# Kernel optimization log

Measured on AMD Instinct MI355X. Metric: run time of the kernel, lower is better.

## Reference

```python
import jax, jax.numpy as jnp
import numpy as np

S, B, E, H = 2048, 2, 1024, 16
D = E // H  # head_dim = 64


def setup_inputs() -> dict:
    key = jax.random.key(0)
    ks = jax.random.split(key, 5)
    sp = (2.0 / (E + E)) ** 0.5  # xavier-ish scale
    return {
        "x": jax.random.normal(ks[0], (S, B, E), dtype=jnp.float32),
        "wq": jax.random.normal(ks[1], (E, E), dtype=jnp.float32) * sp,
        "bq": jnp.zeros((E,), jnp.float32),
        "wk": jax.random.normal(ks[2], (E, E), dtype=jnp.float32) * sp,
        "bk": jnp.zeros((E,), jnp.float32),
        "wv": jax.random.normal(ks[3], (E, E), dtype=jnp.float32) * sp,
        "bv": jnp.zeros((E,), jnp.float32),
        "wo": jax.random.normal(ks[4], (E, E), dtype=jnp.float32) * sp,
        "bo": jnp.zeros((E,), jnp.float32),
    }


def reference(x, wq, bq, wk, bk, wv, bv, wo, bo):
    # x: (S, B, E), weights in torch Linear convention (out, in)
    scaling = jnp.float32(D ** -0.5)
    q = (jnp.einsum('ibe,fe->ibf', x, wq) + bq) * scaling
    k = jnp.einsum('ibe,fe->ibf', x, wk) + bk
    v = jnp.einsum('ibe,fe->ibf', x, wv) + bv
    q = q.reshape(S, B, H, D)
    k = k.reshape(S, B, H, D)
    v = v.reshape(S, B, H, D)
    # energy: (B, H, S_q, S_k)
    energy = jnp.einsum('ibnf,jbnf->bnij', q, k)
    causal = jnp.triu(jnp.ones((S, S), dtype=bool), k=1)  # True above diagonal
    energy = jnp.where(causal[None, None], -jnp.inf, energy)
    weights = jax.nn.softmax(energy, axis=-1)
    head_ctx = jnp.einsum('bnij,jbnf->ibnf', weights, v)
    context = head_ctx.reshape(S, B, E)
    out = jnp.einsum('ibe,fe->ibf', context, wo) + bo
    return out
```

## Files before the change

### kernel.cpp

```cpp
#include <hip/hip_runtime.h>
#include <hip/hip_bf16.h>
#include <stdint.h>

#define S_LEN 2048
#define BATCH 2
#define EMB   1024
#define NH    16
#define HD    64
#define LOG2E 1.4426950408889634f

typedef __bf16 bf16x8 __attribute__((ext_vector_type(8)));
typedef float  f32x4  __attribute__((ext_vector_type(4)));
typedef unsigned short ushort8 __attribute__((ext_vector_type(8)));

__device__ __forceinline__ unsigned short f2bf(float f) {
  __bf16 h = (__bf16)f;
  return __builtin_bit_cast(unsigned short, h);
}

__device__ __forceinline__ ushort8 cvt8(const float4 a, const float4 b) {
  ushort8 o;
  o[0]=f2bf(a.x); o[1]=f2bf(a.y); o[2]=f2bf(a.z); o[3]=f2bf(a.w);
  o[4]=f2bf(b.x); o[5]=f2bf(b.y); o[6]=f2bf(b.z); o[7]=f2bf(b.w);
  return o;
}

__device__ __forceinline__ unsigned long long pack4(const f32x4 v) {
  return  (unsigned long long)f2bf(v[0])
       | ((unsigned long long)f2bf(v[1]) << 16)
       | ((unsigned long long)f2bf(v[2]) << 32)
       | ((unsigned long long)f2bf(v[3]) << 48);
}

#define GLOAD16(g, l) __builtin_amdgcn_global_load_lds( \
    (const __attribute__((address_space(1))) void*)(g),  \
    (__attribute__((address_space(3))) void*)(l), 16, 0, 0)

__global__ __launch_bounds__(256) void k_cvt(const float* __restrict__ src,
                                             unsigned short* __restrict__ dst,
                                             int n) {
  int i = (blockIdx.x*256 + threadIdx.x)*8;
  if (i >= n) return;
  const float4* s4 = (const float4*)(src + i);
  *(ushort8*)(dst + i) = cvt8(s4[0], s4[1]);
}

__global__ __launch_bounds__(256) void k_cvt_all(
    const float* __restrict__ x,
    const float* __restrict__ wq, const float* __restrict__ wk,
    const float* __restrict__ wv,
    unsigned short* __restrict__ xb, unsigned short* __restrict__ wb) {
  const int b = blockIdx.x;
  const float* src;
  unsigned short* dst;
  int off;
  if (b < 2048) { src = x; dst = xb; off = b; }
  else {
    const int t = b - 2048;
    const int z = t >> 9;
    src = (z==0) ? wq : ((z==1) ? wk : wv);
    dst = wb + (size_t)z*EMB*EMB;
    off = t & 511;
  }
  const int i = (off*256 + threadIdx.x)*8;
  const float4* s4 = (const float4*)(src + i);
  *(ushort8*)(dst + i) = cvt8(s4[0], s4[1]);
}

__global__ __launch_bounds__(256) void k_qkv_bb(
    const unsigned short* __restrict__ xb,
    const unsigned short* __restrict__ wb,
    const float* __restrict__ bq, const float* __restrict__ bk,
    const float* __restrict__ bv,
    unsigned short* __restrict__ Qb, unsigned short* __restrict__ Kb,
    unsigned short* __restrict__ Vtb)
{
  __shared__ unsigned short Al[2][128*32];
  __shared__ unsigned short Bl[2][128*32];
  const int tid = threadIdx.x;
  const int lin  = blockIdx.x;
  const int wgid = (lin & 7)*96 + (lin >> 3);
  const int mb   = wgid / 24;
  const int t    = wgid % 24;
  const int z    = t >> 3;
  const int nb   = t & 7;
  const int m0 = mb * 128;
  const int n0 = nb * 128;
  const int w = tid >> 6, lane = tid & 63;
  const int wr = w >> 1, wc = w & 1;
  const int lr = lane & 15, lhi = lane >> 4;
  const unsigned short* wz = wb + (size_t)z * (EMB*EMB);

  const unsigned short* ag[2];
  const unsigned short* bg[2];
  int ub[2];
#pragma unroll
  for (int j=0;j<2;++j) {
    const int c   = j*256 + tid;
    const int row = c >> 2;
    const int col = (c & 3) << 3;
    ag[j] = xb + (size_t)(m0+row)*EMB + col;
    bg[j] = wz + (size_t)(n0+row)*EMB + col;
    ub[j] = (j*256 + (tid & 192)) * 16;
  }

  auto STAGE = [&](int k0, int b2) {
#pragma unroll
    for (int j=0;j<2;++j) {
      GLOAD16(ag[j] + k0, (char*)Al[b2] + ub[j]);
      GLOAD16(bg[j] + k0, (char*)Bl[b2] + ub[j]);
    }
  };

  f32x4 acc[4][4];
#pragma unroll
  for (int m=0;m<4;++m)
#pragma unroll
    for (int n=0;n<4;++n) acc[m][n] = (f32x4){0.f,0.f,0.f,0.f};

  STAGE(0, 0);
  int bbuf = 0;
  for (int k0 = 0; k0 < EMB; k0 += 32) {
    if (k0 + 32 < EMB) {
      STAGE(k0 + 32, bbuf^1);
      asm volatile("s_waitcnt vmcnt(4)" ::: "memory");
    } else {
      asm volatile("s_waitcnt vmcnt(0)" ::: "memory");
    }
    __builtin_amdgcn_s_barrier();

    bf16x8 af[4], bfr[4];
#pragma unroll
    for (int m=0;m<4;++m) af[m]  = *(const bf16x8*)&Al[bbuf][(wr*64 + m*16 + lr)*32 + lhi*8];
#pragma unroll
    for (int n=0;n<4;++n) bfr[n] = *(const bf16x8*)&Bl[bbuf][(wc*64 + n*16 + lr)*32 + lhi*8];
    __builtin_amdgcn_s_setprio(1);
#pragma unroll
    for (int m=0;m<4;++m)
#pragma unroll
      for (int n=0;n<4;++n)
        acc[m][n] = __builtin_amdgcn_mfma_f32_16x16x32_bf16(af[m], bfr[n], acc[m][n], 0,0,0);
    __builtin_amdgcn_s_setprio(0);

    __builtin_amdgcn_s_barrier();
    bbuf ^= 1;
  }

  const float scale = (z==0) ? 0.125f*LOG2E : 1.0f;
  const float* bias = (z==0) ? bq : ((z==1) ? bk : bv);
#pragma unroll
  for (int m=0;m<4;++m)
#pragma unroll
    for (int n=0;n<4;++n)
#pragma unroll
      for (int r=0;r<4;++r) {
        const int rr   = m0 + wr*64 + m*16 + lhi*4 + r;
        const int fcol = n0 + wc*64 + n*16 + lr;
        const float v = (acc[m][n][r] + bias[fcol]) * scale;
        const unsigned short ov = f2bf(v);
        const int i = rr >> 1, bsel = rr & 1;
        const int h = fcol >> 6, d = fcol & 63;
        const int hh = bsel*NH + h;
        if (z == 0)      Qb [((size_t)hh*S_LEN + i)*HD + d] = ov;
        else if (z == 1) Kb [((size_t)hh*S_LEN + i)*HD + d] = ov;
        else             Vtb[((size_t)hh*HD + d)*S_LEN + i] = ov;
      }
}

__global__ __launch_bounds__(256) void k_qkv_bf(
    const unsigned short* __restrict__ xb,
    const float* __restrict__ wq, const float* __restrict__ wk,
    const float* __restrict__ wv,
    const float* __restrict__ bq, const float* __restrict__ bk,
    const float* __restrict__ bv,
    unsigned short* __restrict__ Qb, unsigned short* __restrict__ Kb,
    unsigned short* __restrict__ Vtb)
{
  __shared__ unsigned short Al[128*32];
  __shared__ unsigned short Bl[128*32];
  const int tid = threadIdx.x;
  const int lin  = blockIdx.x;
  const int wgid = (lin & 7)*96 + (lin >> 3);
  const int mb   = wgid / 24;
  const int t    = wgid % 24;
  const int z    = t >> 3;
  const int nb   = t & 7;
  const int m0 = mb * 128;
  const int n0 = nb * 128;
  const int w = tid >> 6, lane = tid & 63;
  const int wr = w >> 1, wc = w & 1;
  const int lr = lane & 15, lhi = lane >> 4;
  const float* wz = (z==0) ? wq : ((z==1) ? wk : wv);

  f32x4 acc[4][4];
#pragma unroll
  for (int m=0;m<4;++m)
#pragma unroll
    for (int n=0;n<4;++n) acc[m][n] = (f32x4){0.f,0.f,0.f,0.f};

  for (int k0 = 0; k0 < EMB; k0 += 32) {
    float4 b0[2], b1[2];
#pragma unroll
    for (int j = 0; j < 2; ++j) {
      const int c   = j*256 + tid;
      const int row = c >> 2;
      const int col = (c & 3) << 3;
      const float* bp = wz + (size_t)(n0+row)*EMB + k0 + col;
      b0[j] = *(const float4*)bp;  b1[j] = *(const float4*)(bp+4);
    }
    __syncthreads();
#pragma unroll
    for (int j = 0; j < 2; ++j) {
      const int c   = j*256 + tid;
      const int row = c >> 2;
      const int col = (c & 3) << 3;
      const int ub  = (j*256 + (tid & 192)) * 16;
      GLOAD16(xb + (size_t)(m0+row)*EMB + k0 + col, (char*)Al + ub);
      *(ushort8*)&Bl[row*32 + col] = cvt8(b0[j], b1[j]);
    }
    __syncthreads();
    bf16x8 af[4], bfr[4];
#pragma unroll
    for (int m=0;m<4;++m) af[m]  = *(const bf16x8*)&Al[(wr*64 + m*16 + lr)*32 + lhi*8];
#pragma unroll
    for (int n=0;n<4;++n) bfr[n] = *(const bf16x8*)&Bl[(wc*64 + n*16 + lr)*32 + lhi*8];
#pragma unroll
    for (int m=0;m<4;++m)
#pragma unroll
      for (int n=0;n<4;++n)
        acc[m][n] = __builtin_amdgcn_mfma_f32_16x16x32_bf16(af[m], bfr[n], acc[m][n], 0,0,0);
  }

  const float scale = (z==0) ? 0.125f*LOG2E : 1.0f;
  const float* bias = (z==0) ? bq : ((z==1) ? bk : bv);
#pragma unroll
  for (int m=0;m<4;++m)
#pragma unroll
    for (int n=0;n<4;++n)
#pragma unroll
      for (int r=0;r<4;++r) {
        const int rr   = m0 + wr*64 + m*16 + lhi*4 + r;
        const int fcol = n0 + wc*64 + n*16 + lr;
        const float v = (acc[m][n][r] + bias[fcol]) * scale;
        const unsigned short ov = f2bf(v);
        const int i = rr >> 1, bsel = rr & 1;
        const int h = fcol >> 6, d = fcol & 63;
        const int hh = bsel*NH + h;
        if (z == 0)      Qb [((size_t)hh*S_LEN + i)*HD + d] = ov;
        else if (z == 1) Kb [((size_t)hh*S_LEN + i)*HD + d] = ov;
        else             Vtb[((size_t)hh*HD + d)*S_LEN + i] = ov;
      }
}

__global__ __launch_bounds__(256) void k_qkv(
    const float* __restrict__ xA, int a_rs, int ishift,
    const float* __restrict__ wq, const float* __restrict__ wk,
    const float* __restrict__ wv,
    const float* __restrict__ bq, const float* __restrict__ bk,
    const float* __restrict__ bv,
    unsigned short* __restrict__ Qb, unsigned short* __restrict__ Kb,
    unsigned short* __restrict__ Vtb)
{
  __shared__ unsigned short Al[128*32];
  __shared__ unsigned short Bl[128*32];
  const int tid = threadIdx.x;
  const int z  = blockIdx.z;
  const int m0 = blockIdx.x * 128;
  const int n0 = blockIdx.y * 128;
  const int w = tid >> 6, lane = tid & 63;
  const int wr = w >> 1, wc = w & 1;
  const int lr = lane & 15, lhi = lane >> 4;
  const float* wz = (z==0) ? wq : ((z==1) ? wk : wv);

  f32x4 acc[4][4];
#pragma unroll
  for (int m=0;m<4;++m)
#pragma unroll
    for (int n=0;n<4;++n) acc[m][n] = (f32x4){0.f,0.f,0.f,0.f};

  for (int k0 = 0; k0 < EMB; k0 += 32) {
    float4 a0[2], a1[2], b0[2], b1[2];
#pragma unroll
    for (int j = 0; j < 2; ++j) {
      const int c   = j*256 + tid;
      const int row = c >> 2;
      const int col = (c & 3) << 3;
      const float* ap = xA + (size_t)(m0+row)*a_rs + k0 + col;
      const float* bp = wz + (size_t)(n0+row)*EMB + k0 + col;
      a0[j] = *(const float4*)ap;  a1[j] = *(const float4*)(ap+4);
      b0[j] = *(const float4*)bp;  b1[j] = *(const float4*)(bp+4);
    }
    __syncthreads();
#pragma unroll
    for (int j = 0; j < 2; ++j) {
      const int c   = j*256 + tid;
      const int row = c >> 2;
      const int col = (c & 3) << 3;
      *(ushort8*)&Al[row*32 + col] = cvt8(a0[j], a1[j]);
      *(ushort8*)&Bl[row*32 + col] = cvt8(b0[j], b1[j]);
    }
    __syncthreads();
    bf16x8 af[4], bfr[4];
#pragma unroll
    for (int m=0;m<4;++m) af[m]  = *(const bf16x8*)&Al[(wr*64 + m*16 + lr)*32 + lhi*8];
#pragma unroll
    for (int n=0;n<4;++n) bfr[n] = *(const bf16x8*)&Bl[(wc*64 + n*16 + lr)*32 + lhi*8];
#pragma unroll
    for (int m=0;m<4;++m)
#pragma unroll
      for (int n=0;n<4;++n)
        acc[m][n] = __builtin_amdgcn_mfma_f32_16x16x32_bf16(af[m], bfr[n], acc[m][n], 0,0,0);
  }

  const float scale = (z==0) ? 0.125f*LOG2E : 1.0f;
  const float* bias = (z==0) ? bq : ((z==1) ? bk : bv);
  const int bmask = (1 << ishift) - 1;
#pragma unroll
  for (int m=0;m<4;++m)
#pragma unroll
    for (int n=0;n<4;++n)
#pragma unroll
      for (int r=0;r<4;++r) {
        const int rr   = m0 + wr*64 + m*16 + lhi*4 + r;
        const int fcol = n0 + wc*64 + n*16 + lr;
        const float v = (acc[m][n][r] + bias[fcol]) * scale;
        const unsigned short ov = f2bf(v);
        const int i = rr >> ishift, bsel = rr & bmask;
        const int h = fcol >> 6, d = fcol & 63;
        const int hh = bsel*NH + h;
        if (z == 0)      Qb [((size_t)hh*S_LEN + i)*HD + d] = ov;
        else if (z == 1) Kb [((size_t)hh*S_LEN + i)*HD + d] = ov;
        else             Vtb[((size_t)hh*HD + d)*S_LEN + i] = ov;
      }
}

__global__ __launch_bounds__(256,4) void k_attn(
    const unsigned short* __restrict__ Q,
    const unsigned short* __restrict__ K,
    const unsigned short* __restrict__ Vt,
    unsigned short* __restrict__ ctx, int bshift, int hsh)
{
  __shared__ unsigned short KL[2][64*64];
  __shared__ unsigned short VL[2][64*64];
  __shared__ unsigned short Pl[4][16*64];

  const int tid = threadIdx.x;
  const int w = tid >> 6, lane = tid & 63;
  const int lr = lane & 15, lhi = lane >> 4;

  const int lin = blockIdx.x;
  const int cc  = lin >> hsh;
  const int chunk = (cc < 16) ? cc : (47 - cc);
  const int hh  = lin & ((1 << hsh) - 1);
  const int q0  = chunk*64 + w*16;

  const unsigned short* Qh = Q  + (size_t)hh*S_LEN*HD;
  const unsigned short* Kh = K  + (size_t)hh*S_LEN*HD;
  const unsigned short* Vh = Vt + (size_t)hh*HD*S_LEN;
  char* Pw = (char*)Pl[w];

  const int xm = (lr & 7) << 4;
  int kvb[2];
#pragma unroll
  for (int kf=0;kf<2;++kf) kvb[kf] = lr*128 + ((kf*64 + lhi*16) ^ xm);
  int pwb[4];
#pragma unroll
  for (int kn=0;kn<4;++kn)
    pwb[kn] = lr*128 + ((kn*32 + lhi*8) ^ xm);

  const unsigned short* kga[2];
  const unsigned short* vga[2];
#pragma unroll
  for (int j=0;j<2;++j) {
    const int c   = j*256 + tid;
    const int row = c >> 3;
    const int sb  = (c*16) ^ ((row & 7) << 4);
    const int el  = (sb & 127) >> 1;
    kga[j] = Kh + (size_t)row*HD + el;
    vga[j] = Vh + (size_t)row*S_LEN + el;
  }
  const int ub0 = (tid & 192) * 16;

  bf16x8 qf[2];
#pragma unroll
  for (int kf=0;kf<2;++kf)
    qf[kf] = *(const bf16x8*)&Qh[(size_t)(q0 + lr)*HD + kf*32 + lhi*8];

  f32x4 o[4];
  float rm = -3.0e38f, rl = 0.f;
#pragma unroll
  for (int dn=0;dn<4;++dn) o[dn] = (f32x4){0.f,0.f,0.f,0.f};

  const int tmax = chunk + 1;

  auto STAGE = [&](int tt, int bb2) {
#pragma unroll
    for (int j=0;j<2;++j) {
      GLOAD16(kga[j] + (size_t)tt*4096, (char*)KL[bb2] + ub0 + j*4096);
      GLOAD16(vga[j] + (size_t)tt*64,   (char*)VL[bb2] + ub0 + j*4096);
    }
  };

  STAGE(0, 0);
  int bb = 0;
  for (int t = 0; t < tmax; ++t) {
    if (t + 1 < tmax) {
      STAGE(t+1, bb^1);
      asm volatile("s_waitcnt vmcnt(4)" ::: "memory");
    } else {
      asm volatile("s_waitcnt vmcnt(0)" ::: "memory");
    }
    __builtin_amdgcn_s_barrier();

    const int kv0 = t*64;
    const char* KB = (const char*)KL[bb];
    const char* VB = (const char*)VL[bb];

    f32x4 st[4];
#pragma unroll
    for (int kn=0;kn<4;++kn) st[kn] = (f32x4){0.f,0.f,0.f,0.f};

    __builtin_amdgcn_s_setprio(1);
#pragma unroll
    for (int kn=0;kn<4;++kn)
#pragma unroll
      for (int kf=0;kf<2;++kf) {
        const bf16x8 kfr = *(const bf16x8*)(KB + kvb[kf] + kn*2048);
        st[kn] = __builtin_amdgcn_mfma_f32_16x16x32_bf16(kfr, qf[kf], st[kn], 0,0,0);
      }
    __builtin_amdgcn_s_setprio(0);

    if (t == tmax-1) {
      const int q = q0 + lr;
#pragma unroll
      for (int kn=0;kn<4;++kn)
#pragma unroll
        for (int r=0;r<4;++r) {
          const int k = kv0 + kn*16 + lhi*4 + r;
          if (k > q) st[kn][r] = -1.0e30f;
        }
    }

    float mx = fmaxf(fmaxf(st[0][0], st[0][1]), fmaxf(st[0][2], st[0][3]));
#pragma unroll
    for (int kn=1;kn<4;++kn)
      mx = fmaxf(mx, fmaxf(fmaxf(st[kn][0], st[kn][1]),
                           fmaxf(st[kn][2], st[kn][3])));
    mx = fmaxf(mx, __shfl_xor(mx, 16));
    mx = fmaxf(mx, __shfl_xor(mx, 32));
    if (!__all(mx - rm <= 8.0f)) {
      const float newm  = fmaxf(rm, mx);
      const float alpha = exp2f(rm - newm);
      rl *= alpha;
#pragma unroll
      for (int dn=0;dn<4;++dn)
#pragma unroll
        for (int r=0;r<4;++r) o[dn][r] *= alpha;
      rm = newm;
    }
    float sum = 0.f;
#pragma unroll
    for (int kn=0;kn<4;++kn)
#pragma unroll
      for (int r=0;r<4;++r) {
        const float p = exp2f(st[kn][r] - rm);
        st[kn][r] = p;
        sum += p;
      }
    sum += __shfl_xor(sum, 16);
    sum += __shfl_xor(sum, 32);
    rl += sum;

#pragma unroll
    for (int kn=0;kn<4;++kn)
      *(unsigned long long*)(Pw + pwb[kn]) = pack4(st[kn]);

#pragma unroll
    for (int ks=0;ks<2;++ks) {
      const bf16x8 pfr = *(const bf16x8*)(Pw + kvb[ks]);
      __builtin_amdgcn_s_setprio(1);
#pragma unroll
      for (int dn=0;dn<4;++dn) {
        const bf16x8 vf = *(const bf16x8*)(VB + kvb[ks] + dn*2048);
        o[dn] = __builtin_amdgcn_mfma_f32_16x16x32_bf16(vf, pfr, o[dn], 0,0,0);
      }
      __builtin_amdgcn_s_setprio(0);
    }

    __builtin_amdgcn_s_barrier();
    bb ^= 1;
  }

  const int h = hh & (NH-1);
  const int badd = hh >> 4;
  const float inv = 1.0f / rl;
  const int q = q0 + lr;
  const size_t trow = ((size_t)q << bshift) + badd;
#pragma unroll
  for (int dn=0;dn<4;++dn) {
    f32x4 ov;
#pragma unroll
    for (int r=0;r<4;++r) ov[r] = o[dn][r]*inv;
    *(unsigned long long*)&ctx[trow*EMB + h*HD + dn*16 + lhi*4] = pack4(ov);
  }
}

__global__ __launch_bounds__(256) void k_oproj_bf(
    const unsigned short* __restrict__ ctxA,
    const unsigned short* __restrict__ wob,
    const float* __restrict__ bo,
    float* __restrict__ out)
{
  __shared__ unsigned short Al[2][128*32];
  __shared__ unsigned short Bl[2][128*32];
  const int tid = threadIdx.x;
  const int m0 = blockIdx.x * 128;
  const int n0 = blockIdx.y * 128;
  const int w = tid >> 6, lane = tid & 63;
  const int wr = w >> 1, wc = w & 1;
  const int lr = lane & 15, lhi = lane >> 4;

  const unsigned short* ag[2];
  const unsigned short* bg[2];
  int ub[2];
#pragma unroll
  for (int j=0;j<2;++j) {
    const int c   = j*256 + tid;
    const int row = c >> 2;
    const int col = (c & 3) << 3;
    ag[j] = ctxA + (size_t)(m0+row)*EMB + col;
    bg[j] = wob  + (size_t)(n0+row)*EMB + col;
    ub[j] = (j*256 + (tid & 192)) * 16;
  }

  auto STAGE = [&](int k0, int b2) {
#pragma unroll
    for (int j=0;j<2;++j) {
      GLOAD16(ag[j] + k0, (char*)Al[b2] + ub[j]);
      GLOAD16(bg[j] + k0, (char*)Bl[b2] + ub[j]);
    }
  };

  f32x4 acc[4][4];
#pragma unroll
  for (int m=0;m<4;++m)
#pragma unroll
    for (int n=0;n<4;++n) acc[m][n] = (f32x4){0.f,0.f,0.f,0.f};

  STAGE(0, 0);
  int bbuf = 0;
  for (int k0 = 0; k0 < EMB; k0 += 32) {
    if (k0 + 32 < EMB) {
      STAGE(k0 + 32, bbuf^1);
      asm volatile("s_waitcnt vmcnt(4)" ::: "memory");
    } else {
      asm volatile("s_waitcnt vmcnt(0)" ::: "memory");
    }
    __builtin_amdgcn_s_barrier();

    bf16x8 af[4], bfr[4];
#pragma unroll
    for (int m=0;m<4;++m) af[m]  = *(const bf16x8*)&Al[bbuf][(wr*64 + m*16 + lr)*32 + lhi*8];
#pragma unroll
    for (int n=0;n<4;++n) bfr[n] = *(const bf16x8*)&Bl[bbuf][(wc*64 + n*16 + lr)*32 + lhi*8];
    __builtin_amdgcn_s_setprio(1);
#pragma unroll
    for (int m=0;m<4;++m)
#pragma unroll
      for (int n=0;n<4;++n)
        acc[m][n] = __builtin_amdgcn_mfma_f32_16x16x32_bf16(af[m], bfr[n], acc[m][n], 0,0,0);
    __builtin_amdgcn_s_setprio(0);

    __builtin_amdgcn_s_barrier();
    bbuf ^= 1;
  }

#pragma unroll
  for (int m=0;m<4;++m)
#pragma unroll
    for (int n=0;n<4;++n)
#pragma unroll
      for (int r=0;r<4;++r) {
        const int rr   = m0 + wr*64 + m*16 + lhi*4 + r;
        const int fcol = n0 + wc*64 + n*16 + lr;
        out[(size_t)rr*EMB + fcol] = acc[m][n][r] + bo[fcol];
      }
}

__global__ __launch_bounds__(256) void k_oproj(
    const unsigned short* __restrict__ ctxA,
    const float* __restrict__ wo,
    const float* __restrict__ bo,
    float* __restrict__ outb, int orm)
{
  __shared__ unsigned short Al[128*32];
  __shared__ unsigned short Bl[128*32];
  const int tid = threadIdx.x;
  const int m0 = blockIdx.x * 128;
  const int n0 = blockIdx.y * 128;
  const int w = tid >> 6, lane = tid & 63;
  const int wr = w >> 1, wc = w & 1;
  const int lr = lane & 15, lhi = lane >> 4;

  f32x4 acc[4][4];
#pragma unroll
  for (int m=0;m<4;++m)
#pragma unroll
    for (int n=0;n<4;++n) acc[m][n] = (f32x4){0.f,0.f,0.f,0.f};

  for (int k0 = 0; k0 < EMB; k0 += 32) {
    float4 b0[2], b1[2];
#pragma unroll
    for (int j = 0; j < 2; ++j) {
      const int c   = j*256 + tid;
      const int row = c >> 2;
      const int col = (c & 3) << 3;
      const float* bp = wo + (size_t)(n0+row)*EMB + k0 + col;
      b0[j] = *(const float4*)bp;  b1[j] = *(const float4*)(bp+4);
    }
    __syncthreads();
#pragma unroll
    for (int j = 0; j < 2; ++j) {
      const int c   = j*256 + tid;
      const int row = c >> 2;
      const int col = (c & 3) << 3;
      const int ub  = (j*256 + (tid & 192)) * 16;
      GLOAD16(ctxA + (size_t)(m0+row)*EMB + k0 + col, (char*)Al + ub);
      *(ushort8*)&Bl[row*32 + col] = cvt8(b0[j], b1[j]);
    }
    __syncthreads();
    bf16x8 af[4], bfr[4];
#pragma unroll
    for (int m=0;m<4;++m) af[m]  = *(const bf16x8*)&Al[(wr*64 + m*16 + lr)*32 + lhi*8];
#pragma unroll
    for (int n=0;n<4;++n) bfr[n] = *(const bf16x8*)&Bl[(wc*64 + n*16 + lr)*32 + lhi*8];
#pragma unroll
    for (int m=0;m<4;++m)
#pragma unroll
      for (int n=0;n<4;++n)
        acc[m][n] = __builtin_amdgcn_mfma_f32_16x16x32_bf16(af[m], bfr[n], acc[m][n], 0,0,0);
  }

#pragma unroll
  for (int m=0;m<4;++m)
#pragma unroll
    for (int n=0;n<4;++n)
#pragma unroll
      for (int r=0;r<4;++r) {
        const int rr   = m0 + wr*64 + m*16 + lhi*4 + r;
        const int fcol = n0 + wc*64 + n*16 + lr;
        outb[(size_t)rr*orm*EMB + fcol] = acc[m][n][r] + bo[fcol];
      }
}

extern "C" void kernel_launch(void* const* d_in, const int* in_sizes, int n_in,
                              void* d_out, int out_size, void* d_ws, size_t ws_size,
                              hipStream_t stream) {
  const float* x  = (const float*)d_in[0];
  const float* wq = (const float*)d_in[1];
  const float* bq = (const float*)d_in[2];
  const float* wk = (const float*)d_in[3];
  const float* bk = (const float*)d_in[4];
  const float* wv = (const float*)d_in[5];
  const float* bv = (const float*)d_in[6];
  const float* wo = (const float*)d_in[7];
  const float* bo = (const float*)d_in[8];
  float* out = (float*)d_out;

  char* ws = (char*)d_ws;
  const size_t MB = (size_t)1 << 20;

  if (ws_size >= 38*MB) {
    unsigned short* Q   = (unsigned short*)(ws + 0*MB);
    unsigned short* K   = (unsigned short*)(ws + 8*MB);
    unsigned short* Vt  = (unsigned short*)(ws + 16*MB);
    unsigned short* wb  = (unsigned short*)(ws + 24*MB);
    unsigned short* xb  = (unsigned short*)(ws + 30*MB);
    unsigned short* cx  = (unsigned short*)(ws + 24*MB);
    unsigned short* wob = Vt;

    k_cvt_all<<<3584, 256, 0, stream>>>(x, wq, wk, wv, xb, wb);
    k_qkv_bb<<<768, 256, 0, stream>>>(xb, wb, bq,bk,bv, Q, K, Vt);
    k_attn<<<1024, 256, 0, stream>>>(Q, K, Vt, cx, 1, 5);
    k_cvt<<<512, 256, 0, stream>>>(wo, wob, EMB*EMB);
    k_oproj_bf<<<dim3(32,8), 256, 0, stream>>>(cx, wob, bo, out);
  } else if (ws_size >= 32*MB) {
    unsigned short* Q   = (unsigned short*)(ws + 0*MB);
    unsigned short* K   = (unsigned short*)(ws + 8*MB);
    unsigned short* Vt  = (unsigned short*)(ws + 16*MB);
    unsigned short* cx  = (unsigned short*)(ws + 24*MB);
    unsigned short* xb  = cx;
    unsigned short* wob = Vt;

    k_cvt<<<2048, 256, 0, stream>>>(x, xb, (S_LEN*BATCH)*EMB);
    k_qkv_bf<<<768, 256, 0, stream>>>(xb, wq,wk,wv, bq,bk,bv, Q, K, Vt);
    k_attn<<<1024, 256, 0, stream>>>(Q, K, Vt, cx, 1, 5);
    k_cvt<<<512, 256, 0, stream>>>(wo, wob, EMB*EMB);
    k_oproj_bf<<<dim3(32,8), 256, 0, stream>>>(cx, wob, bo, out);
  } else {
    unsigned short* Q  = (unsigned short*)(ws + 0*MB);
    unsigned short* K  = (unsigned short*)(ws + 4*MB);
    unsigned short* Vt = (unsigned short*)(ws + 8*MB);
    unsigned short* cx = (unsigned short*)(ws + 12*MB);
    for (int b = 0; b < 2; ++b) {
      k_qkv<<<dim3(16,8,3), 256, 0, stream>>>(x + b*EMB, 2*EMB, 0,
                                              wq,wk,wv, bq,bk,bv, Q,K,Vt);
      k_attn<<<512, 256, 0, stream>>>(Q, K, Vt, cx, 0, 4);
      k_oproj<<<dim3(16,8), 256, 0, stream>>>(cx, wo, bo, out + b*EMB, 2);
    }
  }
}
```

Before: 126.4 us.

## Split long causal attention chunks across two KV halves with a combine pass

The attention kernel is replaced by a variant that splits the KV range of the later query chunks into two halves handled by separate blocks. It stores a normalized partial output plus running max/sum statistics, and a new combine kernel merges the halves into the context buffer. This shortens the longest per-block tile loop and evens out per-block work under the causal mask. The cost is an extra kernel launch, extra global traffic for the partials, and a bf16 rounding of the partial outputs before the merge.

Measured after the change: 132.2 us. +4.5%, slower.

```diff
diff --git a/kernel.cpp b/kernel.cpp
--- a/kernel.cpp
+++ b/kernel.cpp
@@ -16,6 +16,9 @@
 __device__ __forceinline__ unsigned short f2bf(float f) {
   __bf16 h = (__bf16)f;
   return __builtin_bit_cast(unsigned short, h);
+}
+__device__ __forceinline__ float bf2f(unsigned short u) {
+  return (float)__builtin_bit_cast(__bf16, u);
 }
 
 __device__ __forceinline__ ushort8 cvt8(const float4 a, const float4 b) {
@@ -334,7 +337,224 @@
       }
 }
 
-__global__ __launch_bounds__(256,4) void k_attn(
+__global__ __launch_bounds__(256,4) void k_attn_j(
+    const unsigned short* __restrict__ Q,
+    const unsigned short* __restrict__ K,
+    const unsigned short* __restrict__ Vt,
+    unsigned short* __restrict__ ctx,
+    unsigned short* __restrict__ PA,
+    float2* __restrict__ mlA, float2* __restrict__ mlB)
+{
+  __shared__ unsigned short KL[2][64*64];
+  __shared__ unsigned short VL[2][64*64];
+  __shared__ unsigned short Pl[4][16*64];
+
+  const int tid = threadIdx.x;
+  const int w = tid >> 6, lane = tid & 63;
+  const int lr = lane & 15, lhi = lane >> 4;
+
+  const int j  = blockIdx.x >> 5;
+  const int hh = blockIdx.x & 31;
+  int c, ts, nt, mode;
+  if (j < 16)      { c = 31-j; ts = (c+1)>>1; nt = (c+1)-ts; mode = 2; }
+  else if (j < 32) { c = 47-j; ts = 0;        nt = (c+1)>>1; mode = 1; }
+  else             { c = 47-j; ts = 0;        nt = c+1;      mode = 0; }
+  const bool diag = (mode != 1);
+  const int q0 = c*64 + w*16;
+
+  const unsigned short* Qh = Q  + (size_t)hh*S_LEN*HD;
+  const unsigned short* Kh = K  + (size_t)hh*S_LEN*HD;
+  const unsigned short* Vh = Vt + (size_t)hh*HD*S_LEN;
+  char* Pw = (char*)Pl[w];
+
+  const int xm = (lr & 7) << 4;
+  int kvb[2];
+#pragma unroll
+  for (int kf=0;kf<2;++kf) kvb[kf] = lr*128 + ((kf*64 + lhi*16) ^ xm);
+  int pwb[4];
+#pragma unroll
+  for (int kn=0;kn<4;++kn)
+    pwb[kn] = lr*128 + ((kn*32 + lhi*8) ^ xm);
+
+  const unsigned short* kga[2];
+  const unsigned short* vga[2];
+#pragma unroll
+  for (int jj=0;jj<2;++jj) {
+    const int cc  = jj*256 + tid;
+    const int row = cc >> 3;
+    const int sb  = (cc*16) ^ ((row & 7) << 4);
+    const int el  = (sb & 127) >> 1;
+    kga[jj] = Kh + (size_t)row*HD + el;
+    vga[jj] = Vh + (size_t)row*S_LEN + el;
+  }
+  const int ub0 = (tid & 192) * 16;
+
+  bf16x8 qf[2];
+#pragma unroll
+  for (int kf=0;kf<2;++kf)
+    qf[kf] = *(const bf16x8*)&Qh[(size_t)(q0 + lr)*HD + kf*32 + lhi*8];
+
+  f32x4 o[4];
+  float rm = -3.0e38f, rl = 0.f;
+#pragma unroll
+  for (int dn=0;dn<4;++dn) o[dn] = (f32x4){0.f,0.f,0.f,0.f};
+
+  auto STAGE = [&](int tt, int bb2) {
+#pragma unroll
+    for (int jj=0;jj<2;++jj) {
+      GLOAD16(kga[jj] + (size_t)tt*4096, (char*)KL[bb2] + ub0 + jj*4096);
+      GLOAD16(vga[jj] + (size_t)tt*64,   (char*)VL[bb2] + ub0 + jj*4096);
+    }
+  };
+
+  STAGE(ts, 0);
+  int bb = 0;
+  for (int i = 0; i < nt; ++i) {
+    const int t = ts + i;
+    if (i + 1 < nt) {
+      STAGE(t+1, bb^1);
+      asm volatile("s_waitcnt vmcnt(4)" ::: "memory");
+    } else {
+      asm volatile("s_waitcnt vmcnt(0)" ::: "memory");
+    }
+    __builtin_amdgcn_s_barrier();
+
+    const int kv0 = t*64;
+    const char* KB = (const char*)KL[bb];
+    const char* VB = (const char*)VL[bb];
+
+    f32x4 st[4];
+#pragma unroll
+    for (int kn=0;kn<4;++kn) st[kn] = (f32x4){0.f,0.f,0.f,0.f};
+
+    __builtin_amdgcn_s_setprio(1);
+#pragma unroll
+    for (int kn=0;kn<4;++kn)
+#pragma unroll
+      for (int kf=0;kf<2;++kf) {
+        const bf16x8 kfr = *(const bf16x8*)(KB + kvb[kf] + kn*2048);
+        st[kn] = __builtin_amdgcn_mfma_f32_16x16x32_bf16(kfr, qf[kf], st[kn], 0,0,0);
+      }
+    __builtin_amdgcn_s_setprio(0);
+
+    if (diag && i == nt-1) {
+      const int qr = q0 + lr;
+#pragma unroll
+      for (int kn=0;kn<4;++kn)
+#pragma unroll
+        for (int r=0;r<4;++r) {
+          const int k = kv0 + kn*16 + lhi*4 + r;
+          if (k > qr) st[kn][r] = -1.0e30f;
+        }
+    }
+
+    float mx = fmaxf(fmaxf(st[0][0], st[0][1]), fmaxf(st[0][2], st[0][3]));
+#pragma unroll
+    for (int kn=1;kn<4;++kn)
+      mx = fmaxf(mx, fmaxf(fmaxf(st[kn][0], st[kn][1]),
+                           fmaxf(st[kn][2], st[kn][3])));
+    mx = fmaxf(mx, __shfl_xor(mx, 16));
+    mx = fmaxf(mx, __shfl_xor(mx, 32));
+    if (!__all(mx - rm <= 8.0f)) {
+      const float newm  = fmaxf(rm, mx);
+      const float alpha = exp2f(rm - newm);
+      rl *= alpha;
+#pragma unroll
+      for (int dn=0;dn<4;++dn)
+#pragma unroll
+        for (int r=0;r<4;++r) o[dn][r] *= alpha;
+      rm = newm;
+    }
+    float sum = 0.f;
+#pragma unroll
+    for (int kn=0;kn<4;++kn)
+#pragma unroll
+      for (int r=0;r<4;++r) {
+        const float p = exp2f(st[kn][r] - rm);
+        st[kn][r] = p;
+        sum += p;
+      }
+    sum += __shfl_xor(sum, 16);
+    sum += __shfl_xor(sum, 32);
+    rl += sum;
+
+#pragma unroll
+    for (int kn=0;kn<4;++kn)
+      *(unsigned long long*)(Pw + pwb[kn]) = pack4(st[kn]);
+
+#pragma unroll
+    for (int ks=0;ks<2;++ks) {
+      const bf16x8 pfr = *(const bf16x8*)(Pw + kvb[ks]);
+      __builtin_amdgcn_s_setprio(1);
+#pragma unroll
+      for (int dn=0;dn<4;++dn) {
+        const bf16x8 vf = *(const bf16x8*)(VB + kvb[ks] + dn*2048);
+        o[dn] = __builtin_amdgcn_mfma_f32_16x16x32_bf16(vf, pfr, o[dn], 0,0,0);
+      }
+      __builtin_amdgcn_s_setprio(0);
+    }
+
+    __builtin_amdgcn_s_barrier();
+    bb ^= 1;
+  }
+
+  const float inv = 1.0f / rl;
+  const int qr = q0 + lr;
+  if (mode == 1) {
+    unsigned short* pb = PA + (((size_t)hh << 10) + (qr - 1024))*64;
+#pragma unroll
+    for (int dn=0;dn<4;++dn) {
+      f32x4 ov;
+#pragma unroll
+      for (int r=0;r<4;++r) ov[r] = o[dn][r]*inv;
+      *(unsigned long long*)(pb + dn*16 + lhi*4) = pack4(ov);
+    }
+    if (lhi == 0) mlA[((size_t)hh << 10) + (qr - 1024)] = make_float2(rm, rl);
+  } else {
+    const int h = hh & (NH-1);
+    const int badd = hh >> 4;
+    const size_t trow = ((size_t)qr << 1) + badd;
+#pragma unroll
+    for (int dn=0;dn<4;++dn) {
+      f32x4 ov;
+#pragma unroll
+      for (int r=0;r<4;++r) ov[r] = o[dn][r]*inv;
+      *(unsigned long long*)&ctx[trow*EMB + h*HD + dn*16 + lhi*4] = pack4(ov);
+    }
+    if (mode == 2 && lhi == 0)
+      mlB[((size_t)hh << 10) + (qr - 1024)] = make_float2(rm, rl);
+  }
+}
+
+__global__ __launch_bounds__(256) void k_comb(
+    const unsigned short* __restrict__ PA,
+    const float2* __restrict__ mlA, const float2* __restrict__ mlB,
+    unsigned short* __restrict__ ctx)
+{
+  const int gid = blockIdx.x*256 + threadIdx.x;
+  const int hh  = gid >> 13;
+  const int rem = gid & 8191;
+  const int q   = rem >> 3;
+  const int d0  = (rem & 7) << 3;
+  const float2 A = mlA[((size_t)hh << 10) + q];
+  const float2 B = mlB[((size_t)hh << 10) + q];
+  const float m  = fmaxf(A.x, B.x);
+  float wA = exp2f(A.x - m) * A.y;
+  float wB = exp2f(B.x - m) * B.y;
+  const float inv = 1.0f / (wA + wB);
+  wA *= inv;  wB *= inv;
+  const ushort8 a8 = *(const ushort8*)&PA[((((size_t)hh << 10) + q) << 6) + d0];
+  const size_t trow = (size_t)(1024 + q)*2 + (hh >> 4);
+  unsigned short* cp = ctx + trow*EMB + (hh & 15)*HD + d0;
+  const ushort8 b8 = *(const ushort8*)cp;
+  ushort8 r;
+#pragma unroll
+  for (int i=0;i<8;++i)
+    r[i] = f2bf(bf2f(a8[i])*wA + bf2f(b8[i])*wB);
+  *(ushort8*)cp = r;
+}
+
+__global__ __launch_bounds__(256,4) void k_attn_u(
     const unsigned short* __restrict__ Q,
     const unsigned short* __restrict__ K,
     const unsigned short* __restrict__ Vt,
@@ -677,11 +897,15 @@
     unsigned short* wb  = (unsigned short*)(ws + 24*MB);
     unsigned short* xb  = (unsigned short*)(ws + 30*MB);
     unsigned short* cx  = (unsigned short*)(ws + 24*MB);
+    unsigned short* PA  = (unsigned short*)(ws + 32*MB);
+    float2*         mlA = (float2*)(ws + 36*MB);
+    float2*         mlB = (float2*)(ws + 36*MB + 256*1024);
     unsigned short* wob = Vt;
 
     k_cvt_all<<<3584, 256, 0, stream>>>(x, wq, wk, wv, xb, wb);
     k_qkv_bb<<<768, 256, 0, stream>>>(xb, wb, bq,bk,bv, Q, K, Vt);
-    k_attn<<<1024, 256, 0, stream>>>(Q, K, Vt, cx, 1, 5);
+    k_attn_j<<<1536, 256, 0, stream>>>(Q, K, Vt, cx, PA, mlA, mlB);
+    k_comb<<<1024, 256, 0, stream>>>(PA, mlA, mlB, cx);
     k_cvt<<<512, 256, 0, stream>>>(wo, wob, EMB*EMB);
     k_oproj_bf<<<dim3(32,8), 256, 0, stream>>>(cx, wob, bo, out);
   } else if (ws_size >= 32*MB) {
@@ -694,7 +918,7 @@
 
     k_cvt<<<2048, 256, 0, stream>>>(x, xb, (S_LEN*BATCH)*EMB);
     k_qkv_bf<<<768, 256, 0, stream>>>(xb, wq,wk,wv, bq,bk,bv, Q, K, Vt);
-    k_attn<<<1024, 256, 0, stream>>>(Q, K, Vt, cx, 1, 5);
+    k_attn_u<<<1024, 256, 0, stream>>>(Q, K, Vt, cx, 1, 5);
     k_cvt<<<512, 256, 0, stream>>>(wo, wob, EMB*EMB);
     k_oproj_bf<<<dim3(32,8), 256, 0, stream>>>(cx, wob, bo, out);
   } else {
@@ -705,7 +929,7 @@
     for (int b = 0; b < 2; ++b) {
       k_qkv<<<dim3(16,8,3), 256, 0, stream>>>(x + b*EMB, 2*EMB, 0,
                                               wq,wk,wv, bq,bk,bv, Q,K,Vt);
-      k_attn<<<512, 256, 0, stream>>>(Q, K, Vt, cx, 0, 4);
+      k_attn_u<<<512, 256, 0, stream>>>(Q, K, Vt, cx, 0, 4);
       k_oproj<<<dim3(16,8), 256, 0, stream>>>(cx, wo, bo, out + b*EMB, 2);
     }
   }
```

## Fold wo conversion into cvt_all and defer softmax row-sum reduction

Applied to the files above, without the earlier changes.

Adds a 40MB workspace path where the wo weight conversion is folded into the single k_cvt_all launch, writing to its own buffer so one kernel launch is removed. In the attention kernel, the per-tile cross-lane shuffle reduction of the softmax denominator moves to after the loop, with each lane accumulating a partial sum. The max reduction is reshaped into four independent chains, and the bf16 pack now builds 32-bit halves instead of a 64-bit value. This relies on the per-lane partial sums staying consistent under the alpha rescaling, which holds because alpha is wave-uniform.

Result: faster. 122.5 us (-3.1%).

```diff
diff --git a/kernel.cpp b/kernel.cpp
--- a/kernel.cpp
+++ b/kernel.cpp
@@ -25,11 +25,11 @@
   return o;
 }
 
-__device__ __forceinline__ unsigned long long pack4(const f32x4 v) {
-  return  (unsigned long long)f2bf(v[0])
-       | ((unsigned long long)f2bf(v[1]) << 16)
-       | ((unsigned long long)f2bf(v[2]) << 32)
-       | ((unsigned long long)f2bf(v[3]) << 48);
+__device__ __forceinline__ uint2 pack4(const f32x4 v) {
+  uint2 r;
+  r.x = (unsigned)f2bf(v[0]) | ((unsigned)f2bf(v[1]) << 16);
+  r.y = (unsigned)f2bf(v[2]) | ((unsigned)f2bf(v[3]) << 16);
+  return r;
 }
 
 #define GLOAD16(g, l) __builtin_amdgcn_global_load_lds( \
@@ -48,8 +48,9 @@
 __global__ __launch_bounds__(256) void k_cvt_all(
     const float* __restrict__ x,
     const float* __restrict__ wq, const float* __restrict__ wk,
-    const float* __restrict__ wv,
-    unsigned short* __restrict__ xb, unsigned short* __restrict__ wb) {
+    const float* __restrict__ wv, const float* __restrict__ wo,
+    unsigned short* __restrict__ xb, unsigned short* __restrict__ wb,
+    unsigned short* __restrict__ wob) {
   const int b = blockIdx.x;
   const float* src;
   unsigned short* dst;
@@ -58,8 +59,8 @@
   else {
     const int t = b - 2048;
     const int z = t >> 9;
-    src = (z==0) ? wq : ((z==1) ? wk : wv);
-    dst = wb + (size_t)z*EMB*EMB;
+    if (z < 3) { src = (z==0) ? wq : ((z==1) ? wk : wv); dst = wb + (size_t)z*EMB*EMB; }
+    else       { src = wo; dst = wob; }
     off = t & 511;
   }
   const int i = (off*256 + threadIdx.x)*8;
@@ -334,7 +335,7 @@
       }
 }
 
-__global__ __launch_bounds__(256,4) void k_attn(
+__global__ __launch_bounds__(256,4) void k_attn_u(
     const unsigned short* __restrict__ Q,
     const unsigned short* __restrict__ K,
     const unsigned short* __restrict__ Vt,
@@ -441,11 +442,11 @@
         }
     }
 
-    float mx = fmaxf(fmaxf(st[0][0], st[0][1]), fmaxf(st[0][2], st[0][3]));
-#pragma unroll
-    for (int kn=1;kn<4;++kn)
-      mx = fmaxf(mx, fmaxf(fmaxf(st[kn][0], st[kn][1]),
-                           fmaxf(st[kn][2], st[kn][3])));
+    float t0 = fmaxf(fmaxf(fmaxf(st[0][0], st[0][1]), st[0][2]), st[0][3]);
+    float t1 = fmaxf(fmaxf(fmaxf(st[1][0], st[1][1]), st[1][2]), st[1][3]);
+    float t2 = fmaxf(fmaxf(fmaxf(st[2][0], st[2][1]), st[2][2]), st[2][3]);
+    float t3 = fmaxf(fmaxf(fmaxf(st[3][0], st[3][1]), st[3][2]), st[3][3]);
+    float mx = fmaxf(fmaxf(fmaxf(t0, t1), t2), t3);
     mx = fmaxf(mx, __shfl_xor(mx, 16));
     mx = fmaxf(mx, __shfl_xor(mx, 32));
     if (!__all(mx - rm <= 8.0f)) {
@@ -458,22 +459,18 @@
         for (int r=0;r<4;++r) o[dn][r] *= alpha;
       rm = newm;
     }
-    float sum = 0.f;
 #pragma unroll
     for (int kn=0;kn<4;++kn)
 #pragma unroll
       for (int r=0;r<4;++r) {
         const float p = exp2f(st[kn][r] - rm);
         st[kn][r] = p;
-        sum += p;
+        rl += p;
       }
-    sum += __shfl_xor(sum, 16);
-    sum += __shfl_xor(sum, 32);
-    rl += sum;
 
 #pragma unroll
     for (int kn=0;kn<4;++kn)
-      *(unsigned long long*)(Pw + pwb[kn]) = pack4(st[kn]);
+      *(uint2*)(Pw + pwb[kn]) = pack4(st[kn]);
 
 #pragma unroll
     for (int ks=0;ks<2;++ks) {
@@ -491,6 +488,8 @@
     bb ^= 1;
   }
 
+  rl += __shfl_xor(rl, 16);
+  rl += __shfl_xor(rl, 32);
   const int h = hh & (NH-1);
   const int badd = hh >> 4;
   const float inv = 1.0f / rl;
@@ -501,7 +500,7 @@
     f32x4 ov;
 #pragma unroll
     for (int r=0;r<4;++r) ov[r] = o[dn][r]*inv;
-    *(unsigned long long*)&ctx[trow*EMB + h*HD + dn*16 + lhi*4] = pack4(ov);
+    *(uint2*)&ctx[trow*EMB + h*HD + dn*16 + lhi*4] = pack4(ov);
   }
 }
 
@@ -670,7 +669,20 @@
   char* ws = (char*)d_ws;
   const size_t MB = (size_t)1 << 20;
 
-  if (ws_size >= 38*MB) {
+  if (ws_size >= 40*MB) {
+    unsigned short* Q   = (unsigned short*)(ws + 0*MB);
+    unsigned short* K   = (unsigned short*)(ws + 8*MB);
+    unsigned short* Vt  = (unsigned short*)(ws + 16*MB);
+    unsigned short* wb  = (unsigned short*)(ws + 24*MB);
+    unsigned short* xb  = (unsigned short*)(ws + 30*MB);
+    unsigned short* wob = (unsigned short*)(ws + 38*MB);
+    unsigned short* cx  = (unsigned short*)(ws + 24*MB);
+
+    k_cvt_all<<<4096, 256, 0, stream>>>(x, wq, wk, wv, wo, xb, wb, wob);
+    k_qkv_bb<<<768, 256, 0, stream>>>(xb, wb, bq,bk,bv, Q, K, Vt);
+    k_attn_u<<<1024, 256, 0, stream>>>(Q, K, Vt, cx, 1, 5);
+    k_oproj_bf<<<dim3(32,8), 256, 0, stream>>>(cx, wob, bo, out);
+  } else if (ws_size >= 38*MB) {
     unsigned short* Q   = (unsigned short*)(ws + 0*MB);
     unsigned short* K   = (unsigned short*)(ws + 8*MB);
     unsigned short* Vt  = (unsigned short*)(ws + 16*MB);
@@ -679,9 +691,9 @@
     unsigned short* cx  = (unsigned short*)(ws + 24*MB);
     unsigned short* wob = Vt;
 
-    k_cvt_all<<<3584, 256, 0, stream>>>(x, wq, wk, wv, xb, wb);
+    k_cvt_all<<<3584, 256, 0, stream>>>(x, wq, wk, wv, wo, xb, wb, (unsigned short*)0);
     k_qkv_bb<<<768, 256, 0, stream>>>(xb, wb, bq,bk,bv, Q, K, Vt);
-    k_attn<<<1024, 256, 0, stream>>>(Q, K, Vt, cx, 1, 5);
+    k_attn_u<<<1024, 256, 0, stream>>>(Q, K, Vt, cx, 1, 5);
     k_cvt<<<512, 256, 0, stream>>>(wo, wob, EMB*EMB);
     k_oproj_bf<<<dim3(32,8), 256, 0, stream>>>(cx, wob, bo, out);
   } else if (ws_size >= 32*MB) {
@@ -694,7 +706,7 @@
 
     k_cvt<<<2048, 256, 0, stream>>>(x, xb, (S_LEN*BATCH)*EMB);
     k_qkv_bf<<<768, 256, 0, stream>>>(xb, wq,wk,wv, bq,bk,bv, Q, K, Vt);
-    k_attn<<<1024, 256, 0, stream>>>(Q, K, Vt, cx, 1, 5);
+    k_attn_u<<<1024, 256, 0, stream>>>(Q, K, Vt, cx, 1, 5);
     k_cvt<<<512, 256, 0, stream>>>(wo, wob, EMB*EMB);
     k_oproj_bf<<<dim3(32,8), 256, 0, stream>>>(cx, wob, bo, out);
   } else {
@@ -705,7 +717,7 @@
     for (int b = 0; b < 2; ++b) {
       k_qkv<<<dim3(16,8,3), 256, 0, stream>>>(x + b*EMB, 2*EMB, 0,
                                               wq,wk,wv, bq,bk,bv, Q,K,Vt);
-      k_attn<<<512, 256, 0, stream>>>(Q, K, Vt, cx, 0, 4);
+      k_attn_u<<<512, 256, 0, stream>>>(Q, K, Vt, cx, 0, 4);
       k_oproj<<<dim3(16,8), 256, 0, stream>>>(cx, wo, bo, out + b*EMB, 2);
     }
   }
```
